# Kernel tuning notes

Measured on AMD Instinct MI355X. Metric: run time of the kernel, lower is better.

## Reference

```python
import jax, jax.numpy as jnp
import numpy as np

RESO = 32
IMG_RESO = 16
PADDING = 0.1
K = 8
B = 2
N_HEADS = 8
SIGMA = 2.0  # kernel_size default in forward


def _triplane_coords():
    r = jnp.arange(RESO, dtype=jnp.float32)
    mid = (RESO - 1) / 2.0
    X, Z = jnp.meshgrid(r, r)  # indexing='xy' like torch
    xz = jnp.stack([X, jnp.full_like(X, mid), Z], axis=-1)
    X, Y = jnp.meshgrid(r, r)
    xy = jnp.stack([X, Y, jnp.full_like(X, mid)], axis=-1)
    Y, Z = jnp.meshgrid(r, r)
    yz = jnp.stack([jnp.full_like(Y, mid), Y, Z], axis=-1)
    c = jnp.concatenate([xz, xy, yz], axis=0) / (RESO - 1)  # (3*RESO, RESO, 3)
    return (c - 0.5) * 2.0 * (1.0 + PADDING + 1e-5)


def _vit_coords():
    r = jnp.arange(IMG_RESO, dtype=jnp.float32)
    X, Y = jnp.meshgrid(r, r)
    return jnp.stack([X, Y], axis=-1).reshape(IMG_RESO * IMG_RESO, 2)  # (256,2)


def setup_inputs() -> dict:
    key = jax.random.key(0)
    ks = jax.random.split(key, 20)
    s = 0.05
    return {
        'triplane_feat': jax.random.normal(ks[0], (B, 64, 3 * RESO, RESO), jnp.float32),
        'image_feat': jax.random.normal(ks[1], (B, 1280, K, IMG_RESO, IMG_RESO), jnp.float32),
        'proj_mat': jax.random.normal(ks[2], (B, K, 4, 4), jnp.float32),
        'valid_frames': jnp.ones((B, K), jnp.float32),
        'conv_w': jax.random.normal(ks[3], (512, 1280), jnp.float32) * s,
        'conv_b': jax.random.normal(ks[4], (512,), jnp.float32) * s,
        'q_w': jax.random.normal(ks[5], (128, 64), jnp.float32) * s,
        'k_w': jax.random.normal(ks[6], (128, 512), jnp.float32) * s,
        'k_b': jax.random.normal(ks[7], (128,), jnp.float32) * s,
        'v_w': jax.random.normal(ks[8], (128, 512), jnp.float32) * s,
        'v_b': jax.random.normal(ks[9], (128,), jnp.float32) * s,
        'wq': jax.random.normal(ks[10], (128, 128), jnp.float32) * s,
        'wq_b': jax.random.normal(ks[11], (128,), jnp.float32) * s,
        'wk': jax.random.normal(ks[12], (128, 128), jnp.float32) * s,
        'wk_b': jax.random.normal(ks[13], (128,), jnp.float32) * s,
        'wv': jax.random.normal(ks[14], (128, 128), jnp.float32) * s,
        'wv_b': jax.random.normal(ks[15], (128,), jnp.float32) * s,
        'attn_out_w': jax.random.normal(ks[16], (128, 128), jnp.float32) * s,
        'attn_out_b': jax.random.normal(ks[17], (128,), jnp.float32) * s,
        'out_w': jax.random.normal(ks[18], (64, 128), jnp.float32) * s,
        'out_b': jax.random.normal(ks[19], (64,), jnp.float32) * s,
    }


def _forward(triplane_feat, image_feat, proj_mat, valid_frames,
             conv_w, conv_b, q_w, k_w, k_b, v_w, v_b,
             wq, wq_b, wk, wk_b, wv, wv_b, attn_out_w, attn_out_b, out_w, out_b):
    b = triplane_feat.shape[0]
    Nq = 3 * RESO * RESO        # 3072 triplane queries
    Npix = IMG_RESO * IMG_RESO  # 256 tokens per frame

    # 1x1x1 Conv3d == per-channel linear
    img = jnp.einsum('bckhw,oc->bokhw', image_feat, conv_w) + conv_b[None, :, None, None, None]

    # project triplane coords into each image
    tpc = _triplane_coords()                                         # (3R, R, 3)
    homo = jnp.concatenate([tpc, jnp.ones(tpc.shape[:2] + (1,), tpc.dtype)], axis=-1)
    ci = jnp.einsum('hwc,bjkc->bjhwk', homo, proj_mat)               # (B,K,3R,R,4)
    x = ci[..., 0] / ci[..., 2]
    y = ci[..., 1] / ci[..., 2]
    x = x / (224.0 - 1.0) * (IMG_RESO - 1)
    y = y / (224.0 - 1.0) * (IMG_RESO - 1)
    xy = jnp.stack([x, y], axis=-1).reshape(b, K, Nq, 2)             # (B,K,Nq,2)

    # visibility mask via pairwise distance (True == masked out, torch MHA semantics)
    vit = _vit_coords()                                              # (256,2)
    diff = xy[:, :, :, None, :] - vit[None, None, None, :, :]        # (B,K,Nq,256,2)
    dist = jnp.sqrt(jnp.sum(diff * diff, axis=-1))
    mask = dist < SIGMA                                              # (B,K,Nq,256)
    invalid = (1.0 - valid_frames) > 0                               # (B,K)
    mask = jnp.logical_or(mask, invalid[:, :, None, None])
    mask = jnp.transpose(mask, (0, 2, 1, 3)).reshape(b, Nq, K * Npix)

    image_value = img.reshape(b, 512, K * Npix).transpose(0, 2, 1)   # (B,K*256,512)
    triplane_query = triplane_feat.reshape(b, 64, Nq).transpose(0, 2, 1)  # (B,Nq,64)

    q = triplane_query @ q_w.T
    k = image_value @ k_w.T + k_b
    v = image_value @ v_w.T + v_b

    # nn.MultiheadAttention internal projections
    qh = (q @ wq.T + wq_b).reshape(b, Nq, N_HEADS, 128 // N_HEADS)
    kh = (k @ wk.T + wk_b).reshape(b, K * Npix, N_HEADS, 128 // N_HEADS)
    vh = (v @ wv.T + wv_b).reshape(b, K * Npix, N_HEADS, 128 // N_HEADS)
    scale = 1.0 / jnp.sqrt(jnp.asarray(128 // N_HEADS, qh.dtype))
    scores = jnp.einsum('bqhd,bkhd->bhqk', qh * scale, kh)           # (B,H,Nq,Nkv)
    scores = jnp.where(mask[:, None, :, :], -jnp.inf, scores)
    attn_w = jax.nn.softmax(scores, axis=-1)
    attn = jnp.einsum('bhqk,bkhd->bqhd', attn_w, vh).reshape(b, Nq, 128)
    attn = attn @ attn_out_w.T + attn_out_b

    out = attn @ out_w.T + out_b                                     # (B,Nq,64)
    return out.transpose(0, 2, 1).reshape(b, 64, 3 * RESO, RESO)


def reference(triplane_feat, image_feat, proj_mat, valid_frames,
              conv_w, conv_b, q_w, k_w, k_b, v_w, v_b,
              wq, wq_b, wk, wk_b, wv, wv_b, attn_out_w, attn_out_b, out_w, out_b):
    return _forward(triplane_feat, image_feat, proj_mat, valid_frames,
                    conv_w, conv_b, q_w, k_w, k_b, v_w, v_b,
                    wq, wq_b, wk, wk_b, wv, wv_b, attn_out_w, attn_out_b, out_w, out_b)
```

## Files before the change

### kernel.cpp

```cpp
#include <hip/hip_runtime.h>

#define NQ 3072
#define NPIX 256
#define NKV 2048
#define NH 8

typedef __attribute__((ext_vector_type(8))) short short8;
typedef __attribute__((ext_vector_type(16))) float f32x16;

union Frag {
  int4 i;
  short8 s;
  unsigned u[4];
  unsigned short h[8];
};

__device__ inline unsigned short f2bf(float x) {
  unsigned u = __float_as_uint(x);
  return (unsigned short)((u + 0x7FFFu + ((u >> 16) & 1u)) >> 16);
}
__device__ inline unsigned f2bf2(float lo, float hi) {
  unsigned r;
  asm("v_cvt_pk_bf16_f32 %0, %1, %2" : "=v"(r) : "v"(lo), "v"(hi));
  return r;
}
__device__ inline void plswap(unsigned& a, unsigned& b) {
  asm("v_permlane32_swap_b32 %0, %1" : "+v"(a), "+v"(b));
}

#define OFF_TK      0u
#define OFF_TV      65536u
#define OFF_WQ      131072u
#define OFF_WO      139264u
#define OFF_BK1     147456u
#define OFF_BV1     147584u
#define OFF_BO      147712u
#define OFF_WB      147776u
#define OFF_BKF     311616u
#define OFF_BVF     311744u
#define OFF_MB      311872u
#define OFF_QB      705088u
#define OFF_KVP     1098304u
#define OFF_KB      5292608u
#define OFF_VB      5554752u
#define OFF_VT      5816896u
#define OFF_ATTN    6341184u

__global__ __launch_bounds__(256) void k_fuse1(
    const float* __restrict__ wk, const float* __restrict__ k_w,
    const float* __restrict__ wv, const float* __restrict__ v_w,
    const float* __restrict__ wq, const float* __restrict__ q_w,
    const float* __restrict__ out_w, const float* __restrict__ aow,
    const float* __restrict__ k_b, const float* __restrict__ wk_b,
    const float* __restrict__ v_b, const float* __restrict__ wv_b,
    const float* __restrict__ aob, const float* __restrict__ out_b,
    float* __restrict__ ws) {
  int idx = blockIdx.x * 256 + threadIdx.x;
  if (idx < 131072) {
    const float* Wb = (idx < 65536) ? wk : wv;
    const float* Ws = (idx < 65536) ? k_w : v_w;
    float* dst = ws + ((idx < 65536) ? OFF_TK : OFF_TV);
    int t = idx & 65535; int o = t >> 9, m = t & 511;
    float s = 0.f;
#pragma unroll 8
    for (int j = 0; j < 128; ++j) s = fmaf(Wb[o*128+j], Ws[j*512+m], s);
    dst[t] = s;
  } else if (idx < 139264) {
    int t = idx - 131072; int o = t >> 6, c = t & 63;
    float s = 0.f;
#pragma unroll 8
    for (int j = 0; j < 128; ++j) s = fmaf(wq[o*128+j], q_w[j*64+c], s);
    ws[OFF_WQ + t] = s;
  } else if (idx < 147456) {
    int t = idx - 139264; int c = t >> 7, o = t & 127;
    float s = 0.f;
#pragma unroll 8
    for (int j = 0; j < 128; ++j) s = fmaf(out_w[c*128+j], aow[j*128+o], s);
    ws[OFF_WO + t] = s;
  } else if (idx < 147712) {
    int t = idx - 147456; int o = t & 127;
    const float* Wb = (t < 128) ? wk : wv;
    const float* bi = (t < 128) ? k_b : v_b;
    const float* ba = (t < 128) ? wk_b : wv_b;
    float s = 0.f;
    for (int j = 0; j < 128; ++j) s = fmaf(Wb[o*128+j], bi[j], s);
    ws[(t < 128 ? OFF_BK1 : OFF_BV1) + o] = s + ba[o];
  } else if (idx < 147776) {
    int c = idx - 147712;
    float s = 0.f;
    for (int j = 0; j < 128; ++j) s = fmaf(out_w[c*128+j], aob[j], s);
    ws[OFF_BO + c] = s + out_b[c];
  }
}

__global__ __launch_bounds__(256) void k_fuse2(
    const float* __restrict__ Tk, const float* __restrict__ Tv,
    const float* __restrict__ conv_w, unsigned short* __restrict__ WB) {
  __shared__ float Ts[8][512];
  int tid = threadIdx.x;
  const float* T = blockIdx.z ? Tv : Tk;
  int r0 = blockIdx.y * 8;
  for (int i = tid; i < 4096; i += 256) Ts[i >> 9][i & 511] = T[(r0 + (i >> 9))*512 + (i & 511)];
  __syncthreads();
  int c = blockIdx.x * 256 + tid;
  float acc[8] = {0,0,0,0,0,0,0,0};
  for (int m = 0; m < 512; ++m) {
    float w = conv_w[(size_t)m*1280 + c];
#pragma unroll
    for (int r = 0; r < 8; ++r) acc[r] = fmaf(Ts[r][m], w, acc[r]);
  }
#pragma unroll
  for (int r = 0; r < 8; ++r)
    WB[(size_t)(blockIdx.z*128 + r0 + r)*1280 + c] = f2bf(acc[r]);
}

__global__ __launch_bounds__(256) void k_biasf(
    const float* __restrict__ Tk, const float* __restrict__ Tv,
    const float* __restrict__ conv_b, const float* __restrict__ bk1,
    const float* __restrict__ bv1, float* __restrict__ bkf, float* __restrict__ bvf) {
  int tid = threadIdx.x;
  const float* T = (tid < 128) ? Tk : Tv;
  int o = tid & 127;
  float s = 0.f;
  for (int m = 0; m < 512; ++m) s = fmaf(T[o*512+m], conv_b[m], s);
  if (tid < 128) bkf[o] = s + bk1[o]; else bvf[o] = s + bv1[o];
}

__global__ __launch_bounds__(256) void k_maskbits(
    const float* __restrict__ proj, const float* __restrict__ vfr,
    unsigned* __restrict__ MB) {
  int idx = blockIdx.x * 256 + threadIdx.x;
  int q = idx % NQ; int bk = idx / NQ;
  int plane = q >> 10, rem = q & 1023;
  float fi = (float)(rem >> 5), fj = (float)(rem & 31);
  float cx, cy, cz;
  if (plane == 0)      { cx = fj;    cy = 15.5f; cz = fi; }
  else if (plane == 1) { cx = fj;    cy = fi;    cz = 15.5f; }
  else                 { cx = 15.5f; cy = fj;    cz = fi; }
  cx = ((cx / 31.0f) - 0.5f) * 2.0f * 1.10001f;
  cy = ((cy / 31.0f) - 0.5f) * 2.0f * 1.10001f;
  cz = ((cz / 31.0f) - 0.5f) * 2.0f * 1.10001f;
  const float* P = proj + bk * 16;
  float c0 = cx*P[0] + cy*P[1] + cz*P[2] + P[3];
  float c1 = cx*P[4] + cy*P[5] + cz*P[6] + P[7];
  float c2 = cx*P[8] + cy*P[9] + cz*P[10] + P[11];
  float x = (c0 / c2) / 223.0f * 15.0f;
  float y = (c1 / c2) / 223.0f * 15.0f;
  bool invalid = (1.0f - vfr[bk]) > 0.0f;
  unsigned out[8];
#pragma unroll
  for (int w = 0; w < 8; ++w) {
    unsigned word = 0;
#pragma unroll
    for (int i = 0; i < 32; ++i) {
      int p = w*32 + i;
      float dx = x - (float)(p & 15);
      float dy = y - (float)(p >> 4);
      float d2 = fmaf(dx, dx, dy*dy);
      word |= (sqrtf(d2) < 2.0f ? 1u : 0u) << i;
    }
    out[w] = invalid ? 0xFFFFFFFFu : word;
  }
  uint4* dst = (uint4*)(MB + (size_t)idx * 8);
  dst[0] = make_uint4(out[0], out[1], out[2], out[3]);
  dst[1] = make_uint4(out[4], out[5], out[6], out[7]);
}

__global__ __launch_bounds__(256) void k_qh(
    const float* __restrict__ tf, const float* __restrict__ Wq,
    const float* __restrict__ wq_b, unsigned short* __restrict__ QB) {
  __shared__ float A[64][65];
  __shared__ float W[128][65];
  int b = blockIdx.y, q0 = blockIdx.x * 64, tid = threadIdx.x;
  for (int i = tid; i < 4096; i += 256) A[i >> 6][i & 63] = tf[((size_t)(b*64) + (i >> 6))*NQ + q0 + (i & 63)];
  for (int i = tid; i < 8192; i += 256) W[i >> 6][i & 63] = Wq[i];
  __syncthreads();
  int og = tid & 15, qg = tid >> 4;
  float acc[4][8] = {};
  for (int c = 0; c < 64; ++c) {
    float a[4];
#pragma unroll
    for (int jq = 0; jq < 4; ++jq) a[jq] = A[c][qg*4 + jq];
#pragma unroll
    for (int jo = 0; jo < 8; ++jo) {
      float w = W[og*8 + jo][c];
#pragma unroll
      for (int jq = 0; jq < 4; ++jq) acc[jq][jo] = fmaf(a[jq], w, acc[jq][jo]);
    }
  }
#pragma unroll
  for (int jq = 0; jq < 4; ++jq) {
    float v[8];
#pragma unroll
    for (int jo = 0; jo < 8; ++jo) v[jo] = (acc[jq][jo] + wq_b[og*8 + jo]) * 0.25f;
    uint4 pk;
    pk.x = (unsigned)f2bf(v[0]) | ((unsigned)f2bf(v[1]) << 16);
    pk.y = (unsigned)f2bf(v[2]) | ((unsigned)f2bf(v[3]) << 16);
    pk.z = (unsigned)f2bf(v[4]) | ((unsigned)f2bf(v[5]) << 16);
    pk.w = (unsigned)f2bf(v[6]) | ((unsigned)f2bf(v[7]) << 16);
    *(uint4*)(QB + ((size_t)(b*NQ) + q0 + qg*4 + jq)*128 + og*8) = pk;
  }
}

__global__ __launch_bounds__(256, 2) void k_kvhM(
    const float* __restrict__ X, const unsigned short* __restrict__ WB,
    float* __restrict__ KVP) {
  __shared__ float XS[16][32];
  int tid = threadIdx.x;
  int t0  = blockIdx.x * 32;
  int chq = blockIdx.y;
  int b   = blockIdx.z;
  int cb0 = chq * 320;
  int wid = tid >> 6, lane = tid & 63, l32 = lane & 31, hi = lane >> 5;
  f32x16 acc0, acc1;
#pragma unroll
  for (int i = 0; i < 16; ++i) { acc0[i] = 0.f; acc1[i] = 0.f; }
  int ot0 = wid * 2, ot1 = wid * 2 + 1;
  for (int ch = 0; ch < 20; ++ch) {
    int cg0 = cb0 + ch * 16;
    __syncthreads();
    {
      int v = tid;
      XS[v >> 5][v & 31] = X[((size_t)b*1280 + cg0 + (v >> 5))*NKV + t0 + (v & 31)];
      v = tid + 256;
      XS[v >> 5][v & 31] = X[((size_t)b*1280 + cg0 + (v >> 5))*NKV + t0 + (v & 31)];
    }
    __syncthreads();
    Frag fa0, fa1, fb;
    fa0.i = *(const int4*)(WB + (size_t)(ot0*32 + l32)*1280 + cg0 + hi*8);
    fa1.i = *(const int4*)(WB + (size_t)(ot1*32 + l32)*1280 + cg0 + hi*8);
#pragma unroll
    for (int j = 0; j < 4; ++j)
      fb.u[j] = f2bf2(XS[hi*8 + 2*j][l32], XS[hi*8 + 2*j + 1][l32]);
    acc0 = __builtin_amdgcn_mfma_f32_32x32x16_bf16(fa0.s, fb.s, acc0, 0, 0, 0);
    acc1 = __builtin_amdgcn_mfma_f32_32x32x16_bf16(fa1.s, fb.s, acc1, 0, 0, 0);
  }
  float* dst = KVP + ((size_t)(chq*2 + b)*NKV + t0 + l32)*256;
#pragma unroll
  for (int qd = 0; qd < 4; ++qd) {
    *(float4*)(dst + ot0*32 + qd*8 + hi*4) =
        make_float4(acc0[qd*4+0], acc0[qd*4+1], acc0[qd*4+2], acc0[qd*4+3]);
    *(float4*)(dst + ot1*32 + qd*8 + hi*4) =
        make_float4(acc1[qd*4+0], acc1[qd*4+1], acc1[qd*4+2], acc1[qd*4+3]);
  }
}

__global__ __launch_bounds__(256) void k_kvcomb(
    const float* __restrict__ KVP, const float* __restrict__ bkf,
    const float* __restrict__ bvf, unsigned short* __restrict__ KB,
    unsigned short* __restrict__ VB) {
  int idx = blockIdx.x * 256 + threadIdx.x;
  int og4 = idx & 63; int bt = idx >> 6;
  int b = bt >> 11, t = bt & 2047;
  int o0 = og4 * 4;
  float4 s = make_float4(0.f, 0.f, 0.f, 0.f);
#pragma unroll
  for (int ch = 0; ch < 4; ++ch) {
    float4 p = *(const float4*)(KVP + ((size_t)(ch*2 + b)*NKV + t)*256 + o0);
    s.x += p.x; s.y += p.y; s.z += p.z; s.w += p.w;
  }
  if (o0 < 128) {
    float4 bb = *(const float4*)(bkf + o0);
    s.x += bb.x; s.y += bb.y; s.z += bb.z; s.w += bb.w;
    uint2 pk;
    pk.x = (unsigned)f2bf(s.x) | ((unsigned)f2bf(s.y) << 16);
    pk.y = (unsigned)f2bf(s.z) | ((unsigned)f2bf(s.w) << 16);
    *(uint2*)(KB + (size_t)bt*128 + o0) = pk;
  } else {
    int o = o0 - 128;
    float4 bb = *(const float4*)(bvf + o);
    s.x += bb.x; s.y += bb.y; s.z += bb.z; s.w += bb.w;
    uint2 pk;
    pk.x = (unsigned)f2bf(s.x) | ((unsigned)f2bf(s.y) << 16);
    pk.y = (unsigned)f2bf(s.z) | ((unsigned)f2bf(s.w) << 16);
    *(uint2*)(VB + (size_t)bt*128 + o) = pk;
  }
}

__global__ __launch_bounds__(256) void k_vt(
    const unsigned short* __restrict__ VB, unsigned short* __restrict__ VT) {
  __shared__ unsigned short LT[16][264];
  int f = blockIdx.x, b = blockIdx.y, h = blockIdx.z;
  int tid = threadIdx.x;
  {
    const unsigned short* src = VB + ((size_t)(b*NKV) + f*256 + tid)*128 + h*16;
    Frag u1, u2;
    u1.i = *(const int4*)(src);
    u2.i = *(const int4*)(src + 8);
#pragma unroll
    for (int j = 0; j < 8; ++j) { LT[j][tid] = u1.h[j]; LT[8 + j][tid] = u2.h[j]; }
  }
  __syncthreads();
  int row = tid >> 3, pb = (tid & 7) * 32;
  unsigned ow[16];
#pragma unroll
  for (int j = 0; j < 16; ++j) {
    unsigned short v0, v1;
    if (row < 16)       { v0 = LT[row][pb + 2*j]; v1 = LT[row][pb + 2*j + 1]; }
    else if (row == 16) { v0 = 0x3F80; v1 = 0x3F80; }
    else                { v0 = 0; v1 = 0; }
    ow[j] = (unsigned)v0 | ((unsigned)v1 << 16);
  }
  unsigned short* dst = VT + (((size_t)(b*8 + f)*8 + h)*8192 + row*256 + pb);
  *(uint4*)(dst +  0) = make_uint4(ow[0],  ow[1],  ow[2],  ow[3]);
  *(uint4*)(dst +  8) = make_uint4(ow[4],  ow[5],  ow[6],  ow[7]);
  *(uint4*)(dst + 16) = make_uint4(ow[8],  ow[9],  ow[10], ow[11]);
  *(uint4*)(dst + 24) = make_uint4(ow[12], ow[13], ow[14], ow[15]);
}

__global__ __launch_bounds__(256, 3) void k_attnM(
    const unsigned short* __restrict__ QB, const unsigned short* __restrict__ KB,
    const unsigned short* __restrict__ VT, const unsigned* __restrict__ MB,
    float* __restrict__ ATTN) {
  __shared__ float MRG[2][32][32];
  int tid = threadIdx.x;
  int wid = tid >> 6, lane = tid & 63, l32 = lane & 31, hi = lane >> 5;
  int bh = blockIdx.y, b = bh >> 3, h = bh & 7;
  int qts = wid >> 1, ph = wid & 1;
  int qbase = (blockIdx.x * 2 + qts) * 32;
  int ph4 = ph * 4;

  Frag fq;
  fq.i = *(const int4*)(QB + ((size_t)(b*NQ) + qbase + l32)*128 + h*16 + hi*8);

  f32x16 acc;
#pragma unroll
  for (int i = 0; i < 16; ++i) acc[i] = 0.f;
  f32x16 zz;
#pragma unroll
  for (int i = 0; i < 16; ++i) zz[i] = 0.f;

  for (int f = 0; f < 8; ++f) {
    uint4 mv = *(const uint4*)(MB + ((size_t)((b*8 + f)*NQ) + qbase + l32)*8 + ph4);
    unsigned mwa[4] = {mv.x, mv.y, mv.z, mv.w};
    const unsigned short* KBf = KB + ((size_t)(b*NKV) + f*256)*128 + h*16;
    const unsigned short* VTf = VT + (((size_t)(b*8 + f)*8 + h)*8192) + l32*256;
#pragma unroll
    for (int c = 0; c < 4; ++c) {
      int cg = ph4 + c;
      Frag fk;
      fk.i = *(const int4*)(KBf + (size_t)(cg*32 + l32)*128 + hi*8);
      f32x16 S = __builtin_amdgcn_mfma_f32_32x32x16_bf16(fk.s, fq.s, zz, 0, 0, 0);
      unsigned w = mwa[c];
      float e[16];
#pragma unroll
      for (int r = 0; r < 16; ++r) {
        int rl = (r & 3) + 8*(r >> 2) + 4*hi;
        e[r] = ((w >> rl) & 1u) ? 0.f : __expf(S[r]);
      }
#pragma unroll
      for (int half = 0; half < 2; ++half) {
        int e0 = half * 8;
        unsigned x0 = f2bf2(e[e0+0], e[e0+1]);
        unsigned y0 = f2bf2(e[e0+4], e[e0+5]);
        plswap(x0, y0);
        unsigned x1 = f2bf2(e[e0+2], e[e0+3]);
        unsigned y1 = f2bf2(e[e0+6], e[e0+7]);
        plswap(x1, y1);
        Frag fp; fp.u[0] = x0; fp.u[1] = x1; fp.u[2] = y0; fp.u[3] = y1;
        Frag fv;
        fv.i = *(const int4*)(VTf + cg*32 + half*16 + hi*8);
        acc = __builtin_amdgcn_mfma_f32_32x32x16_bf16(fv.s, fp.s, acc, 0, 0, 0);
      }
    }
  }
  if (ph == 1) {
#pragma unroll
    for (int r = 0; r < 16; ++r) {
      int dp = (r & 3) + 8*(r >> 2) + 4*hi;
      MRG[qts][dp][l32] = acc[r];
    }
  }
  __syncthreads();
  if (ph == 0) {
#pragma unroll
    for (int r = 0; r < 16; ++r) {
      int dp = (r & 3) + 8*(r >> 2) + 4*hi;
      acc[r] += MRG[qts][dp][l32];
    }
    float l = __shfl(acc[8], l32);
    float inv = 1.0f / l;
    float* Ap = ATTN + ((size_t)(b*NQ) + qbase + l32)*128 + h*16;
    *(float4*)(Ap + 4*hi)     = make_float4(acc[0]*inv, acc[1]*inv, acc[2]*inv, acc[3]*inv);
    *(float4*)(Ap + 8 + 4*hi) = make_float4(acc[4]*inv, acc[5]*inv, acc[6]*inv, acc[7]*inv);
  }
}

__global__ __launch_bounds__(256) void k_out(
    const float* __restrict__ ATTN, const float* __restrict__ Wo,
    const float* __restrict__ bo, float* __restrict__ out) {
  __shared__ float A[64][129];
  __shared__ float W[64][129];
  int b = blockIdx.y, n0 = blockIdx.x * 64, tid = threadIdx.x;
  for (int i = tid; i < 8192; i += 256) { int n = i >> 7, o = i & 127; A[n][o] = ATTN[((size_t)(b*NQ) + n0 + n)*128 + o]; }
  for (int i = tid; i < 8192; i += 256) { int c = i >> 7, o = i & 127; W[c][o] = Wo[i]; }
  __syncthreads();
  int ng = tid & 31, cg = tid >> 5;
  float acc[2][8] = {};
  for (int o = 0; o < 128; ++o) {
    float a0 = A[ng][o], a1 = A[ng + 32][o];
#pragma unroll
    for (int jc = 0; jc < 8; ++jc) {
      float w = W[cg*8 + jc][o];
      acc[0][jc] = fmaf(a0, w, acc[0][jc]);
      acc[1][jc] = fmaf(a1, w, acc[1][jc]);
    }
  }
#pragma unroll
  for (int jn = 0; jn < 2; ++jn)
#pragma unroll
    for (int jc = 0; jc < 8; ++jc) {
      int c = cg*8 + jc;
      out[((size_t)(b*64) + c)*NQ + n0 + ng + 32*jn] = acc[jn][jc] + bo[c];
    }
}

extern "C" void kernel_launch(void* const* d_in, const int* in_sizes, int n_in,
                              void* d_out, int out_size, void* d_ws, size_t ws_size,
                              hipStream_t stream) {
  const float* tf     = (const float*)d_in[0];
  const float* imf    = (const float*)d_in[1];
  const float* proj   = (const float*)d_in[2];
  const float* vfr    = (const float*)d_in[3];
  const float* conv_w = (const float*)d_in[4];
  const float* conv_b = (const float*)d_in[5];
  const float* q_w    = (const float*)d_in[6];
  const float* k_w    = (const float*)d_in[7];
  const float* k_b    = (const float*)d_in[8];
  const float* v_w    = (const float*)d_in[9];
  const float* v_b    = (const float*)d_in[10];
  const float* wq     = (const float*)d_in[11];
  const float* wq_b   = (const float*)d_in[12];
  const float* wk     = (const float*)d_in[13];
  const float* wk_b   = (const float*)d_in[14];
  const float* wv     = (const float*)d_in[15];
  const float* wv_b   = (const float*)d_in[16];
  const float* aow    = (const float*)d_in[17];
  const float* aob    = (const float*)d_in[18];
  const float* out_w  = (const float*)d_in[19];
  const float* out_b  = (const float*)d_in[20];
  float* ws  = (float*)d_ws;
  float* out = (float*)d_out;
  unsigned short* WB = (unsigned short*)(ws + OFF_WB);
  unsigned short* QB = (unsigned short*)(ws + OFF_QB);
  unsigned short* KB = (unsigned short*)(ws + OFF_KB);
  unsigned short* VB = (unsigned short*)(ws + OFF_VB);
  unsigned short* VT = (unsigned short*)(ws + OFF_VT);
  unsigned* MB = (unsigned*)(ws + OFF_MB);

  k_fuse1<<<dim3(578), dim3(256), 0, stream>>>(wk, k_w, wv, v_w, wq, q_w, out_w, aow,
                                               k_b, wk_b, v_b, wv_b, aob, out_b, ws);
  k_fuse2<<<dim3(5,16,2), dim3(256), 0, stream>>>(ws+OFF_TK, ws+OFF_TV, conv_w, WB);
  k_biasf<<<dim3(1), dim3(256), 0, stream>>>(ws+OFF_TK, ws+OFF_TV, conv_b, ws+OFF_BK1, ws+OFF_BV1,
                                             ws+OFF_BKF, ws+OFF_BVF);
  k_maskbits<<<dim3(192), dim3(256), 0, stream>>>(proj, vfr, MB);
  k_qh<<<dim3(48,2), dim3(256), 0, stream>>>(tf, ws+OFF_WQ, wq_b, QB);
  k_kvhM<<<dim3(64,4,2), dim3(256), 0, stream>>>(imf, WB, ws+OFF_KVP);
  k_kvcomb<<<dim3(1024), dim3(256), 0, stream>>>(ws+OFF_KVP, ws+OFF_BKF, ws+OFF_BVF, KB, VB);
  k_vt<<<dim3(8,2,8), dim3(256), 0, stream>>>(VB, VT);
  k_attnM<<<dim3(48,16), dim3(256), 0, stream>>>(QB, KB, VT, MB, ws+OFF_ATTN);
  k_out<<<dim3(48,2), dim3(256), 0, stream>>>(ws+OFF_ATTN, ws+OFF_WO, ws+OFF_BO, out);
}
```

Baseline: 286.7 us.

## Split conv-weight fusion GEMM over K with partial sums and combine pass

The weight-fusion product (T @ conv_w) moves from 160 blocks, each looping over all 512 reduction steps, to 640 blocks. Each new block handles 16 rows by 64 columns over half of the reduction dimension and writes fp32 partial sums to a new workspace region. A new kernel then adds the two halves and converts the result to bf16. The aim is more parallelism and occupancy for a small GEMM that left most CUs idle, at the cost of an extra launch and an fp32 partial-sum round trip through memory.

```diff
diff --git a/kernel.cpp b/kernel.cpp
--- a/kernel.cpp
+++ b/kernel.cpp
@@ -45,6 +45,7 @@
 #define OFF_VB      5554752u
 #define OFF_VT      5816896u
 #define OFF_ATTN    6341184u
+#define OFF_WP      7127616u
 
 __global__ __launch_bounds__(256) void k_fuse1(
     const float* __restrict__ wk, const float* __restrict__ k_w,
@@ -93,25 +94,54 @@
   }
 }
 
-__global__ __launch_bounds__(256) void k_fuse2(
+__global__ __launch_bounds__(256) void k_fuse2p(
     const float* __restrict__ Tk, const float* __restrict__ Tv,
-    const float* __restrict__ conv_w, unsigned short* __restrict__ WB) {
-  __shared__ float Ts[8][512];
+    const float* __restrict__ conv_w, float* __restrict__ WP) {
+  __shared__ float Ts[256][20];
   int tid = threadIdx.x;
-  const float* T = blockIdx.z ? Tv : Tk;
-  int r0 = blockIdx.y * 8;
-  for (int i = tid; i < 4096; i += 256) Ts[i >> 9][i & 511] = T[(r0 + (i >> 9))*512 + (i & 511)];
+  int x = blockIdx.x, y = blockIdx.y, ks = blockIdx.z;
+  const float* T = (y < 8) ? (Tk + (y*16)*512) : (Tv + ((y-8)*16)*512);
+#pragma unroll
+  for (int k = 0; k < 16; ++k) {
+    int i = tid + k*256;
+    int m = i & 255, r = i >> 8;
+    Ts[m][r] = T[r*512 + ks*256 + m];
+  }
   __syncthreads();
-  int c = blockIdx.x * 256 + tid;
-  float acc[8] = {0,0,0,0,0,0,0,0};
-  for (int m = 0; m < 512; ++m) {
-    float w = conv_w[(size_t)m*1280 + c];
-#pragma unroll
-    for (int r = 0; r < 8; ++r) acc[r] = fmaf(Ts[r][m], w, acc[r]);
-  }
-#pragma unroll
-  for (int r = 0; r < 8; ++r)
-    WB[(size_t)(blockIdx.z*128 + r0 + r)*1280 + c] = f2bf(acc[r]);
+  int col = x*64 + (tid & 63);
+  int rgrp = (tid >> 6) * 4;
+  float acc0=0.f, acc1=0.f, acc2=0.f, acc3=0.f;
+  const float* cw = conv_w + (size_t)(ks*256)*1280 + col;
+  for (int m4 = 0; m4 < 64; ++m4) {
+    float w0 = cw[(size_t)(m4*4+0)*1280];
+    float w1 = cw[(size_t)(m4*4+1)*1280];
+    float w2 = cw[(size_t)(m4*4+2)*1280];
+    float w3 = cw[(size_t)(m4*4+3)*1280];
+    float4 a0 = *(const float4*)&Ts[m4*4+0][rgrp];
+    float4 a1 = *(const float4*)&Ts[m4*4+1][rgrp];
+    float4 a2 = *(const float4*)&Ts[m4*4+2][rgrp];
+    float4 a3 = *(const float4*)&Ts[m4*4+3][rgrp];
+    acc0 = fmaf(a3.x,w3,fmaf(a2.x,w2,fmaf(a1.x,w1,fmaf(a0.x,w0,acc0))));
+    acc1 = fmaf(a3.y,w3,fmaf(a2.y,w2,fmaf(a1.y,w1,fmaf(a0.y,w0,acc1))));
+    acc2 = fmaf(a3.z,w3,fmaf(a2.z,w2,fmaf(a1.z,w1,fmaf(a0.z,w0,acc2))));
+    acc3 = fmaf(a3.w,w3,fmaf(a2.w,w2,fmaf(a1.w,w1,fmaf(a0.w,w0,acc3))));
+  }
+  float* dst = WP + ((size_t)(ks*256 + y*16 + rgrp))*1280 + col;
+  dst[0]    = acc0;
+  dst[1280] = acc1;
+  dst[2560] = acc2;
+  dst[3840] = acc3;
+}
+
+__global__ __launch_bounds__(256) void k_wcomb(
+    const float* __restrict__ WP, unsigned short* __restrict__ WB) {
+  int idx = blockIdx.x * 256 + threadIdx.x;
+  int c2 = idx % 640, r = idx / 640;
+  size_t o = (size_t)r*1280 + c2*2;
+  float2 p0 = *(const float2*)(WP + o);
+  float2 p1 = *(const float2*)(WP + 327680 + o);
+  unsigned pk = (unsigned)f2bf(p0.x + p1.x) | ((unsigned)f2bf(p0.y + p1.y) << 16);
+  *(unsigned*)(WB + o) = pk;
 }
 
 __global__ __launch_bounds__(256) void k_biasf(
@@ -450,7 +480,8 @@
 
   k_fuse1<<<dim3(578), dim3(256), 0, stream>>>(wk, k_w, wv, v_w, wq, q_w, out_w, aow,
                                                k_b, wk_b, v_b, wv_b, aob, out_b, ws);
-  k_fuse2<<<dim3(5,16,2), dim3(256), 0, stream>>>(ws+OFF_TK, ws+OFF_TV, conv_w, WB);
+  k_fuse2p<<<dim3(20,16,2), dim3(256), 0, stream>>>(ws+OFF_TK, ws+OFF_TV, conv_w, ws+OFF_WP);
+  k_wcomb<<<dim3(640), dim3(256), 0, stream>>>(ws+OFF_WP, WB);
   k_biasf<<<dim3(1), dim3(256), 0, stream>>>(ws+OFF_TK, ws+OFF_TV, conv_b, ws+OFF_BK1, ws+OFF_BV1,
                                              ws+OFF_BKF, ws+OFF_BVF);
   k_maskbits<<<dim3(192), dim3(256), 0, stream>>>(proj, vfr, MB);
```

Measured after the change: 253.5 us. -11.6%, faster.
